# Kernel tuning notes

Hardware: AMD Instinct MI355X
Metric: run time of the kernel (lower is better)

Reference implementation:

```python
import jax, jax.numpy as jnp
import numpy as np

MARGIN = 0.5  # hardcoded in the torch __init__ regardless of the margin arg
P_IDS, K_PER_ID, K_PER_MOD = 32, 8, 4
B, C = P_IDS * K_PER_ID, 1024


def setup_inputs() -> dict:
    key = jax.random.key(0)
    inputs = jax.random.normal(key, (B, C), dtype=jnp.float32)
    # Standard cross-modal ReID sampler: P identities, K instances each,
    # first K/2 from modality 0, last K/2 from modality 1. This guarantees the
    # boolean-mask reshape in the original code is well-formed (M per row).
    targets = jnp.repeat(jnp.arange(P_IDS, dtype=jnp.int32), K_PER_ID)
    subs = jnp.tile(jnp.repeat(jnp.arange(2, dtype=jnp.int32), K_PER_MOD), P_IDS)
    return {"inputs": inputs, "targets": targets, "subs": subs, "m_count": K_PER_MOD}


def _loss(inputs, targets, subs, m_count):
    b, c = inputs.shape
    # Mask construction uses detached inputs in the original (clone().detach()).
    xs = jax.lax.stop_gradient(inputs)
    diff = jnp.abs(xs[:, None, :] - xs[None, :, :])                     # (B,B,C)
    identity_mask = targets[:, None] == targets[None, :]                # (B,B)
    modality_mask = subs[:, None] == subs[None, :]                      # (B,B)
    combined = identity_mask & modality_mask                            # (B,B)

    # diff[combined].reshape(B, M, C): every row has exactly m_count trues;
    # stable argsort recovers the selected column indices in ascending order,
    # matching torch's row-major boolean-mask gather.
    order = jnp.argsort(jnp.where(combined, 0, 1), axis=1)              # stable
    idx = order[:, :m_count]                                            # (B,M)
    modality_diff = jnp.take_along_axis(diff, idx[:, :, None], axis=1)  # (B,M,C)

    mean_md = modality_diff.mean(-1, keepdims=True)                     # (B,M,1)
    m_counts = (modality_diff < mean_md * MARGIN).sum(1)                # (B,C) int
    # mdm[i,j,c] = m_counts[i,c] * m_counts[j,c]  (detached float mask)
    mdm = (m_counts[:, None, :] * m_counts[None, :, :]).astype(inputs.dtype)  # (B,B,C)

    mean_d = diff.mean(-1, keepdims=True)                               # (B,B,1)
    idm = (diff < mean_d * MARGIN).astype(inputs.dtype)                 # (B,B,C)

    # Gradient-carrying pairwise differences (vectorized form of the B-loop).
    d = inputs[:, None, :] - inputs[None, :, :]                         # (B,B,C)
    mod_dist = jnp.sqrt(jnp.maximum(((d * mdm) ** 2).sum(-1), 1e-12))   # (B,B)
    id_dist = jnp.sqrt(jnp.maximum(((d * idm) ** 2).sum(-1), 1e-12))    # (B,B)
    id_dist = jnp.where(identity_mask, jnp.inf, id_dist)                # drop same-id

    per_row = jnp.maximum(mod_dist.max(axis=1) * 10.0 - id_dist.min(axis=1), 0.0)
    return per_row.mean()


def reference(inputs, targets, subs, m_count):
    return _loss(inputs, targets, subs, m_count)
```

## Files before the change

kernel.cpp:

```cpp
#include <hip/hip_runtime.h>
#include <math.h>

#define BB 256
#define CC 1024
#define CC4 (CC/4)
#define MARGIN 0.5f
#define NTILE 64
#define JPT 4
#define NP  128

__global__ __launch_bounds__(64) void mcsq_kernel(
    const float* __restrict__ x, const int* __restrict__ targets,
    const int* __restrict__ subs, const int* __restrict__ m_count_p,
    float* __restrict__ mcsq, float* __restrict__ acc,
    unsigned int* __restrict__ cnt_g)
{
    const int i = blockIdx.x;
    const int lane = threadIdx.x;
    if (i == 0 && lane == 0) { *acc = 0.f; *cnt_g = 0u; }
    const int ti = targets[i], si = subs[i];
    int mc = *m_count_p;
    if (mc > 8) mc = 8;

    unsigned long long masks[4];
    #pragma unroll
    for (int q = 0; q < 4; ++q) {
        const int j = q * 64 + lane;
        masks[q] = __ballot(targets[j] == ti && subs[j] == si);
    }
    int idx[8];
    int cnt = 0;
    for (int q = 0; q < 4 && cnt < mc; ++q) {
        unsigned long long m = masks[q];
        while (m && cnt < mc) {
            const int b = __ffsll(m) - 1;
            idx[cnt++] = q * 64 + b;
            m &= m - 1;
        }
    }
    for (int q = 0; q < 4 && cnt < mc; ++q) {
        unsigned long long m = ~masks[q];
        while (m && cnt < mc) {
            const int b = __ffsll(m) - 1;
            idx[cnt++] = q * 64 + b;
            m &= m - 1;
        }
    }

    const float4* x4 = (const float4*)x;
    float4 xi[4];
    #pragma unroll
    for (int t = 0; t < 4; ++t) xi[t] = x4[(long)i * CC4 + lane + 64 * t];

    float4 c4[4];
    #pragma unroll
    for (int t = 0; t < 4; ++t) c4[t] = make_float4(0.f, 0.f, 0.f, 0.f);

    for (int k = 0; k < cnt; ++k) {
        float4 ad[4];
        float s = 0.f;
        #pragma unroll
        for (int t = 0; t < 4; ++t) {
            const float4 xj = x4[(long)idx[k] * CC4 + lane + 64 * t];
            ad[t].x = fabsf(xi[t].x - xj.x);
            ad[t].y = fabsf(xi[t].y - xj.y);
            ad[t].z = fabsf(xi[t].z - xj.z);
            ad[t].w = fabsf(xi[t].w - xj.w);
            s += ad[t].x + ad[t].y + ad[t].z + ad[t].w;
        }
        #pragma unroll
        for (int off = 32; off > 0; off >>= 1) s += __shfl_xor(s, off, 64);
        const float thr = s * (MARGIN / CC);
        #pragma unroll
        for (int t = 0; t < 4; ++t) {
            c4[t].x += (ad[t].x < thr) ? 1.f : 0.f;
            c4[t].y += (ad[t].y < thr) ? 1.f : 0.f;
            c4[t].z += (ad[t].z < thr) ? 1.f : 0.f;
            c4[t].w += (ad[t].w < thr) ? 1.f : 0.f;
        }
    }
    float4* m4 = (float4*)mcsq;
    #pragma unroll
    for (int t = 0; t < 4; ++t) {
        float4 o;
        o.x = c4[t].x * c4[t].x;
        o.y = c4[t].y * c4[t].y;
        o.z = c4[t].z * c4[t].z;
        o.w = c4[t].w * c4[t].w;
        m4[(long)i * CC4 + lane + 64 * t] = o;
    }
}

__global__ __launch_bounds__(256) void pair_kernel(
    const float* __restrict__ x, const float* __restrict__ mcsq,
    const int* __restrict__ targets,
    float* __restrict__ pmax, float* __restrict__ pmin,
    float* __restrict__ pmaxT, float* __restrict__ pminT)
{
    const int tid  = threadIdx.x;
    const int lane = tid & 63;
    const int gw   = blockIdx.x * 4 + (tid >> 6);

    int h = (int)((129.0f - sqrtf(16641.0f - 4.0f * (float)gw)) * 0.5f);
    if (h > 63) h = 63;
    if (h < 0) h = 0;
    while (h > 0 && (129 * h - h * h) > gw) --h;
    while ((129 * (h + 1) - (h + 1) * (h + 1)) <= gw) ++h;
    const int r     = gw - (129 * h - h * h);
    const int cnt_h = 64 - h;
    const int p     = 2 * h + r / cnt_h;
    const int jt    = h + r % cnt_h;

    const int i0 = 2 * p, i1 = 2 * p + 1;

    const float4* x4 = (const float4*)x;
    const float4* m4 = (const float4*)mcsq;

    float4 xi0[4], xi1[4], mi0[4], mi1[4];
    #pragma unroll
    for (int t = 0; t < 4; ++t) {
        const int c4 = lane + 64 * t;
        xi0[t] = x4[(long)i0 * CC4 + c4];
        xi1[t] = x4[(long)i1 * CC4 + c4];
        mi0[t] = m4[(long)i0 * CC4 + c4];
        mi1[t] = m4[(long)i1 * CC4 + c4];
    }
    const int t0 = targets[i0], t1 = targets[i1];

    float max0 = 0.f, max1 = 0.f;
    float min0 = INFINITY, min1 = INFINITY;

    for (int jj = 0; jj < JPT; ++jj) {
        const int j = jt * JPT + jj;
        float4 xa[4], ma[4];
        float s0 = 0.f, s1 = 0.f;
        #pragma unroll
        for (int t = 0; t < 4; ++t) {
            const int c4 = lane + 64 * t;
            xa[t] = x4[(long)j * CC4 + c4];
            ma[t] = m4[(long)j * CC4 + c4];
            s0 += fabsf(xi0[t].x - xa[t].x) + fabsf(xi0[t].y - xa[t].y)
                + fabsf(xi0[t].z - xa[t].z) + fabsf(xi0[t].w - xa[t].w);
            s1 += fabsf(xi1[t].x - xa[t].x) + fabsf(xi1[t].y - xa[t].y)
                + fabsf(xi1[t].z - xa[t].z) + fabsf(xi1[t].w - xa[t].w);
        }
        #pragma unroll
        for (int off = 32; off > 0; off >>= 1) {
            s0 += __shfl_xor(s0, off, 64);
            s1 += __shfl_xor(s1, off, 64);
        }
        const float thr0 = s0 * (MARGIN / CC);
        const float thr1 = s1 * (MARGIN / CC);

        float ids0 = 0.f, ids1 = 0.f, md0 = 0.f, md1 = 0.f;
        #pragma unroll
        for (int t = 0; t < 4; ++t) {
            #pragma unroll
            for (int u = 0; u < 4; ++u) {
                const float xav = (&xa[t].x)[u];
                const float mav = (&ma[t].x)[u];
                const float d0 = (&xi0[t].x)[u] - xav;
                const float q0 = d0 * d0;
                ids0 += (fabsf(d0) < thr0) ? q0 : 0.f;
                md0  += q0 * (&mi0[t].x)[u] * mav;
                const float d1 = (&xi1[t].x)[u] - xav;
                const float q1 = d1 * d1;
                ids1 += (fabsf(d1) < thr1) ? q1 : 0.f;
                md1  += q1 * (&mi1[t].x)[u] * mav;
            }
        }
        #pragma unroll
        for (int off = 32; off > 0; off >>= 1) {
            ids0 += __shfl_xor(ids0, off, 64);
            ids1 += __shfl_xor(ids1, off, 64);
            md0  += __shfl_xor(md0,  off, 64);
            md1  += __shfl_xor(md1,  off, 64);
        }
        const float mod0 = sqrtf(fmaxf(md0, 1e-12f));
        const float mod1 = sqrtf(fmaxf(md1, 1e-12f));
        max0 = fmaxf(max0, mod0);
        max1 = fmaxf(max1, mod1);
        float id0 = sqrtf(fmaxf(ids0, 1e-12f));
        float id1 = sqrtf(fmaxf(ids1, 1e-12f));
        const int tj = targets[j];
        if (tj != t0) min0 = fminf(min0, id0); else id0 = INFINITY;
        if (tj != t1) min1 = fminf(min1, id1); else id1 = INFINITY;
        if (lane == 0) {
            pmaxT[j * NP + p] = fmaxf(mod0, mod1);
            pminT[j * NP + p] = fminf(id0, id1);
        }
    }
    if (lane == 0) {
        pmax[i0 * NTILE + jt] = max0;
        pmax[i1 * NTILE + jt] = max1;
        pmin[i0 * NTILE + jt] = min0;
        pmin[i1 * NTILE + jt] = min1;
    }
}

__global__ __launch_bounds__(64) void final_kernel(
    const float* __restrict__ pmax, const float* __restrict__ pmin,
    const float* __restrict__ pmaxT, const float* __restrict__ pminT,
    float* __restrict__ acc, unsigned int* __restrict__ cnt_g,
    float* __restrict__ out)
{
    const int i = blockIdx.x;
    const int lane = threadIdx.x;
    const int s = i >> 2;
    float mx = 0.f, mn = INFINITY;
    const int t = s + lane;
    if (t < NTILE) {
        mx = fmaxf(mx, pmax[i * NTILE + t]);
        mn = fminf(mn, pmin[i * NTILE + t]);
    }
    const int pv = 2 * s + 2;
    if (lane < pv) {
        mx = fmaxf(mx, pmaxT[i * NP + lane]);
        mn = fminf(mn, pminT[i * NP + lane]);
    }
    if (lane + 64 < pv) {
        mx = fmaxf(mx, pmaxT[i * NP + lane + 64]);
        mn = fminf(mn, pminT[i * NP + lane + 64]);
    }
    #pragma unroll
    for (int off = 32; off > 0; off >>= 1) {
        mx = fmaxf(mx, __shfl_xor(mx, off, 64));
        mn = fminf(mn, __shfl_xor(mn, off, 64));
    }
    if (lane == 0) {
        const float per = fmaxf(mx * 10.f - mn, 0.f);
        atomicAdd(acc, per * (1.0f / BB));
        __threadfence();
        const unsigned int old = atomicAdd(cnt_g, 1u);
        if (old == BB - 1) {
            __threadfence();
            out[0] = atomicAdd(acc, 0.0f);
        }
    }
}

extern "C" void kernel_launch(void* const* d_in, const int* in_sizes, int n_in,
                              void* d_out, int out_size, void* d_ws, size_t ws_size,
                              hipStream_t stream)
{
    const float* x       = (const float*)d_in[0];
    const int*   targets = (const int*)d_in[1];
    const int*   subs    = (const int*)d_in[2];
    const int*   m_count = (const int*)d_in[3];
    float* out  = (float*)d_out;

    float* mcsq  = (float*)d_ws;
    float* pmax  = mcsq  + (long)BB * CC;
    float* pmin  = pmax  + BB * NTILE;
    float* pmaxT = pmin  + BB * NTILE;
    float* pminT = pmaxT + BB * NP;
    float* acc   = pminT + BB * NP;
    unsigned int* cnt_g = (unsigned int*)(acc + 1);

    mcsq_kernel <<<BB,   64, 0, stream>>>(x, targets, subs, m_count, mcsq, acc, cnt_g);
    pair_kernel <<<1040, 256, 0, stream>>>(x, mcsq, targets, pmax, pmin, pmaxT, pminT);
    final_kernel<<<BB,   64, 0, stream>>>(pmax, pmin, pmaxT, pminT, acc, cnt_g, out);
}
```

Measured before the change: 95.57 us.

## Stage j-tile rows in LDS and assign one i-row per wave

The pair kernel's work decomposition changes. Each block now covers a triangular (i-group of 4 rows, j-tile of 4 columns) pair, and each wave handles a single i row instead of two. The four j rows of x and mcsq are loaded cooperatively into 32KB of shared memory, so the four waves reuse them without each fetching them from global memory. The grid doubles to 2080 blocks and the transposed partial buffers grow to BB×BB. The trade is less register reuse of j data across two i rows, in exchange for more parallelism and lower register pressure.

```diff
diff --git a/kernel.cpp b/kernel.cpp
--- a/kernel.cpp
+++ b/kernel.cpp
@@ -7,7 +7,6 @@
 #define MARGIN 0.5f
 #define NTILE 64
 #define JPT 4
-#define NP  128
 
 __global__ __launch_bounds__(64) void mcsq_kernel(
     const float* __restrict__ x, const int* __restrict__ targets,
@@ -99,102 +98,110 @@
 {
     const int tid  = threadIdx.x;
     const int lane = tid & 63;
-    const int gw   = blockIdx.x * 4 + (tid >> 6);
-
-    int h = (int)((129.0f - sqrtf(16641.0f - 4.0f * (float)gw)) * 0.5f);
-    if (h > 63) h = 63;
-    if (h < 0) h = 0;
-    while (h > 0 && (129 * h - h * h) > gw) --h;
-    while ((129 * (h + 1) - (h + 1) * (h + 1)) <= gw) ++h;
-    const int r     = gw - (129 * h - h * h);
-    const int cnt_h = 64 - h;
-    const int p     = 2 * h + r / cnt_h;
-    const int jt    = h + r % cnt_h;
-
-    const int i0 = 2 * p, i1 = 2 * p + 1;
+    const int w    = tid >> 6;
+    const int b    = blockIdx.x;
+
+    int jt = (int)((sqrtf(8.0f * (float)b + 1.0f) - 1.0f) * 0.5f);
+    if (jt < 0) jt = 0;
+    if (jt > 63) jt = 63;
+    while (jt > 0 && (jt * (jt + 1)) / 2 > b) --jt;
+    while (((jt + 1) * (jt + 2)) / 2 <= b) ++jt;
+    const int ig = b - (jt * (jt + 1)) / 2;
+    const int i  = ig * 4 + w;
+    const int j0 = jt * JPT;
+
+    __shared__ float lds[8192];
+    float4* lds4 = (float4*)lds;
 
     const float4* x4 = (const float4*)x;
     const float4* m4 = (const float4*)mcsq;
 
-    float4 xi0[4], xi1[4], mi0[4], mi1[4];
+    const int ti = targets[i];
+    int tj[4];
+    #pragma unroll
+    for (int q = 0; q < 4; ++q) tj[q] = targets[j0 + q];
+
+    float4 xi[4], mi[4];
     #pragma unroll
     for (int t = 0; t < 4; ++t) {
         const int c4 = lane + 64 * t;
-        xi0[t] = x4[(long)i0 * CC4 + c4];
-        xi1[t] = x4[(long)i1 * CC4 + c4];
-        mi0[t] = m4[(long)i0 * CC4 + c4];
-        mi1[t] = m4[(long)i1 * CC4 + c4];
-    }
-    const int t0 = targets[i0], t1 = targets[i1];
-
-    float max0 = 0.f, max1 = 0.f;
-    float min0 = INFINITY, min1 = INFINITY;
-
+        xi[t] = x4[(long)i * CC4 + c4];
+        mi[t] = m4[(long)i * CC4 + c4];
+    }
+
+    {
+        float4 st[8];
+        #pragma unroll
+        for (int q = 0; q < 4; ++q) {
+            st[q]     = x4[(long)(j0 + q) * CC4 + tid];
+            st[4 + q] = m4[(long)(j0 + q) * CC4 + tid];
+        }
+        #pragma unroll
+        for (int q = 0; q < 8; ++q) lds4[q * 256 + tid] = st[q];
+    }
+    __syncthreads();
+
+    const float4* lx = lds4;
+    const float4* lm = lds4 + 1024;
+
+    float mx = 0.f, mn = INFINITY;
+
+    #pragma unroll
     for (int jj = 0; jj < JPT; ++jj) {
-        const int j = jt * JPT + jj;
-        float4 xa[4], ma[4];
-        float s0 = 0.f, s1 = 0.f;
-        #pragma unroll
-        for (int t = 0; t < 4; ++t) {
-            const int c4 = lane + 64 * t;
-            xa[t] = x4[(long)j * CC4 + c4];
-            ma[t] = m4[(long)j * CC4 + c4];
-            s0 += fabsf(xi0[t].x - xa[t].x) + fabsf(xi0[t].y - xa[t].y)
-                + fabsf(xi0[t].z - xa[t].z) + fabsf(xi0[t].w - xa[t].w);
-            s1 += fabsf(xi1[t].x - xa[t].x) + fabsf(xi1[t].y - xa[t].y)
-                + fabsf(xi1[t].z - xa[t].z) + fabsf(xi1[t].w - xa[t].w);
-        }
-        #pragma unroll
-        for (int off = 32; off > 0; off >>= 1) {
-            s0 += __shfl_xor(s0, off, 64);
-            s1 += __shfl_xor(s1, off, 64);
-        }
-        const float thr0 = s0 * (MARGIN / CC);
-        const float thr1 = s1 * (MARGIN / CC);
-
-        float ids0 = 0.f, ids1 = 0.f, md0 = 0.f, md1 = 0.f;
+        const int j = j0 + jj;
+
+        float4 xa[4];
+        float s = 0.f;
+        #pragma unroll
+        for (int t = 0; t < 4; ++t) {
+            xa[t] = lx[jj * 256 + lane + 64 * t];
+            s += fabsf(xi[t].x - xa[t].x) + fabsf(xi[t].y - xa[t].y)
+               + fabsf(xi[t].z - xa[t].z) + fabsf(xi[t].w - xa[t].w);
+        }
+
+        float4 ma[4];
+        #pragma unroll
+        for (int t = 0; t < 4; ++t) ma[t] = lm[jj * 256 + lane + 64 * t];
+
+        #pragma unroll
+        for (int off = 32; off > 0; off >>= 1) s += __shfl_xor(s, off, 64);
+        const float thr = s * (MARGIN / CC);
+
+        float ids = 0.f, md = 0.f;
         #pragma unroll
         for (int t = 0; t < 4; ++t) {
             #pragma unroll
             for (int u = 0; u < 4; ++u) {
+                const float xiv = (&xi[t].x)[u];
+                const float miv = (&mi[t].x)[u];
                 const float xav = (&xa[t].x)[u];
                 const float mav = (&ma[t].x)[u];
-                const float d0 = (&xi0[t].x)[u] - xav;
-                const float q0 = d0 * d0;
-                ids0 += (fabsf(d0) < thr0) ? q0 : 0.f;
-                md0  += q0 * (&mi0[t].x)[u] * mav;
-                const float d1 = (&xi1[t].x)[u] - xav;
-                const float q1 = d1 * d1;
-                ids1 += (fabsf(d1) < thr1) ? q1 : 0.f;
-                md1  += q1 * (&mi1[t].x)[u] * mav;
+                const float d = xiv - xav;
+                const float q = d * d;
+                ids += (fabsf(d) < thr) ? q : 0.f;
+                md  += q * miv * mav;
             }
         }
         #pragma unroll
         for (int off = 32; off > 0; off >>= 1) {
-            ids0 += __shfl_xor(ids0, off, 64);
-            ids1 += __shfl_xor(ids1, off, 64);
-            md0  += __shfl_xor(md0,  off, 64);
-            md1  += __shfl_xor(md1,  off, 64);
-        }
-        const float mod0 = sqrtf(fmaxf(md0, 1e-12f));
-        const float mod1 = sqrtf(fmaxf(md1, 1e-12f));
-        max0 = fmaxf(max0, mod0);
-        max1 = fmaxf(max1, mod1);
-        float id0 = sqrtf(fmaxf(ids0, 1e-12f));
-        float id1 = sqrtf(fmaxf(ids1, 1e-12f));
-        const int tj = targets[j];
-        if (tj != t0) min0 = fminf(min0, id0); else id0 = INFINITY;
-        if (tj != t1) min1 = fminf(min1, id1); else id1 = INFINITY;
+            ids += __shfl_xor(ids, off, 64);
+            md  += __shfl_xor(md,  off, 64);
+        }
+
+        const float mod = sqrtf(fmaxf(md, 1e-12f));
+        float idv = sqrtf(fmaxf(ids, 1e-12f));
+        mx = fmaxf(mx, mod);
+        if (tj[jj] != ti) mn = fminf(mn, idv); else idv = INFINITY;
+
         if (lane == 0) {
-            pmaxT[j * NP + p] = fmaxf(mod0, mod1);
-            pminT[j * NP + p] = fminf(id0, id1);
-        }
-    }
+            pmaxT[j * BB + i] = mod;
+            pminT[j * BB + i] = idv;
+        }
+    }
+
     if (lane == 0) {
-        pmax[i0 * NTILE + jt] = max0;
-        pmax[i1 * NTILE + jt] = max1;
-        pmin[i0 * NTILE + jt] = min0;
-        pmin[i1 * NTILE + jt] = min1;
+        pmax[i * NTILE + jt] = mx;
+        pmin[i * NTILE + jt] = mn;
     }
 }
 
@@ -213,14 +220,14 @@
         mx = fmaxf(mx, pmax[i * NTILE + t]);
         mn = fminf(mn, pmin[i * NTILE + t]);
     }
-    const int pv = 2 * s + 2;
-    if (lane < pv) {
-        mx = fmaxf(mx, pmaxT[i * NP + lane]);
-        mn = fminf(mn, pminT[i * NP + lane]);
-    }
-    if (lane + 64 < pv) {
-        mx = fmaxf(mx, pmaxT[i * NP + lane + 64]);
-        mn = fminf(mn, pminT[i * NP + lane + 64]);
+    const int pv = 4 * s + 4;
+    #pragma unroll
+    for (int q = 0; q < 4; ++q) {
+        const int c = lane + 64 * q;
+        if (c < pv) {
+            mx = fmaxf(mx, pmaxT[i * BB + c]);
+            mn = fminf(mn, pminT[i * BB + c]);
+        }
     }
     #pragma unroll
     for (int off = 32; off > 0; off >>= 1) {
@@ -253,11 +260,11 @@
     float* pmax  = mcsq  + (long)BB * CC;
     float* pmin  = pmax  + BB * NTILE;
     float* pmaxT = pmin  + BB * NTILE;
-    float* pminT = pmaxT + BB * NP;
-    float* acc   = pminT + BB * NP;
+    float* pminT = pmaxT + BB * BB;
+    float* acc   = pminT + BB * BB;
     unsigned int* cnt_g = (unsigned int*)(acc + 1);
 
     mcsq_kernel <<<BB,   64, 0, stream>>>(x, targets, subs, m_count, mcsq, acc, cnt_g);
-    pair_kernel <<<1040, 256, 0, stream>>>(x, mcsq, targets, pmax, pmin, pmaxT, pminT);
+    pair_kernel <<<2080, 256, 0, stream>>>(x, mcsq, targets, pmax, pmin, pmaxT, pminT);
     final_kernel<<<BB,   64, 0, stream>>>(pmax, pmin, pmaxT, pminT, acc, cnt_g, out);
 }
```

Measured after the change: 89.04 us. -6.8%, faster.

## Process two j-tiles per wave, use DPP reductions, halve pair grid

Applied to the files above, without the earlier changes.

Each wavefront in pair_kernel now handles two consecutive j-tiles instead of one. This reuses the i-row registers (xi, mi) across twice the work and halves the grid from 1040 to 528 blocks, with a new triangular index mapping. Wave reductions replace most shuffle-xor steps with DPP row operations plus readfirstlane, and the mcsq loads are issued after the L1 sum so they overlap. Launch bounds now request 4 blocks per CU. The costs are fewer waves to hide latency and a serial loop to compute the tile index.

```diff
diff --git a/kernel.cpp b/kernel.cpp
--- a/kernel.cpp
+++ b/kernel.cpp
@@ -8,6 +8,22 @@
 #define NTILE 64
 #define JPT 4
 #define NP  128
+
+template<int CTRL>
+__device__ __forceinline__ float dpp_add(float v) {
+    const int pi = __builtin_amdgcn_update_dpp(
+        0, __float_as_int(v), CTRL, 0xF, 0xF, false);
+    return v + __int_as_float(pi);
+}
+__device__ __forceinline__ float wred(float v) {
+    v += __shfl_xor(v, 32, 64);
+    v += __shfl_xor(v, 16, 64);
+    v = dpp_add<0x128>(v);
+    v = dpp_add<0x124>(v);
+    v = dpp_add<0x4E>(v);
+    v = dpp_add<0xB1>(v);
+    return __int_as_float(__builtin_amdgcn_readfirstlane(__float_as_int(v)));
+}
 
 __global__ __launch_bounds__(64) void mcsq_kernel(
     const float* __restrict__ x, const int* __restrict__ targets,
@@ -91,7 +107,7 @@
     }
 }
 
-__global__ __launch_bounds__(256) void pair_kernel(
+__global__ __launch_bounds__(256, 4) void pair_kernel(
     const float* __restrict__ x, const float* __restrict__ mcsq,
     const int* __restrict__ targets,
     float* __restrict__ pmax, float* __restrict__ pmin,
@@ -99,17 +115,19 @@
 {
     const int tid  = threadIdx.x;
     const int lane = tid & 63;
-    const int gw   = blockIdx.x * 4 + (tid >> 6);
-
-    int h = (int)((129.0f - sqrtf(16641.0f - 4.0f * (float)gw)) * 0.5f);
-    if (h > 63) h = 63;
-    if (h < 0) h = 0;
-    while (h > 0 && (129 * h - h * h) > gw) --h;
-    while ((129 * (h + 1) - (h + 1) * (h + 1)) <= gw) ++h;
-    const int r     = gw - (129 * h - h * h);
-    const int cnt_h = 64 - h;
-    const int p     = 2 * h + r / cnt_h;
-    const int jt    = h + r % cnt_h;
+    const int W    = blockIdx.x * 4 + (tid >> 6);
+
+    int h = 0, C = 0;
+    while (true) {
+        const int c2 = 2 * ((65 - h) >> 1);
+        if (C + c2 > W) break;
+        C += c2; ++h;
+    }
+    const int ch  = (65 - h) >> 1;
+    const int r   = W - C;
+    const int p   = 2 * h + ((r >= ch) ? 1 : 0);
+    const int rc  = (r >= ch) ? (r - ch) : r;
+    const int jt0 = h + 2 * rc;
 
     const int i0 = 2 * p, i1 = 2 * p + 1;
 
@@ -127,74 +145,78 @@
     }
     const int t0 = targets[i0], t1 = targets[i1];
 
-    float max0 = 0.f, max1 = 0.f;
-    float min0 = INFINITY, min1 = INFINITY;
-
-    for (int jj = 0; jj < JPT; ++jj) {
-        const int j = jt * JPT + jj;
-        float4 xa[4], ma[4];
-        float s0 = 0.f, s1 = 0.f;
-        #pragma unroll
-        for (int t = 0; t < 4; ++t) {
-            const int c4 = lane + 64 * t;
-            xa[t] = x4[(long)j * CC4 + c4];
-            ma[t] = m4[(long)j * CC4 + c4];
-            s0 += fabsf(xi0[t].x - xa[t].x) + fabsf(xi0[t].y - xa[t].y)
-                + fabsf(xi0[t].z - xa[t].z) + fabsf(xi0[t].w - xa[t].w);
-            s1 += fabsf(xi1[t].x - xa[t].x) + fabsf(xi1[t].y - xa[t].y)
-                + fabsf(xi1[t].z - xa[t].z) + fabsf(xi1[t].w - xa[t].w);
-        }
-        #pragma unroll
-        for (int off = 32; off > 0; off >>= 1) {
-            s0 += __shfl_xor(s0, off, 64);
-            s1 += __shfl_xor(s1, off, 64);
-        }
-        const float thr0 = s0 * (MARGIN / CC);
-        const float thr1 = s1 * (MARGIN / CC);
-
-        float ids0 = 0.f, ids1 = 0.f, md0 = 0.f, md1 = 0.f;
-        #pragma unroll
-        for (int t = 0; t < 4; ++t) {
+    #pragma unroll
+    for (int q = 0; q < 2; ++q) {
+        const int jt = jt0 + q;
+        if (jt > 63) break;
+
+        float max0 = 0.f, max1 = 0.f;
+        float min0 = INFINITY, min1 = INFINITY;
+
+        #pragma unroll
+        for (int jj = 0; jj < JPT; ++jj) {
+            const int j = jt * JPT + jj;
+
+            float4 xa[4], ma[4];
+            float s0 = 0.f, s1 = 0.f;
             #pragma unroll
-            for (int u = 0; u < 4; ++u) {
-                const float xav = (&xa[t].x)[u];
-                const float mav = (&ma[t].x)[u];
-                const float d0 = (&xi0[t].x)[u] - xav;
-                const float q0 = d0 * d0;
-                ids0 += (fabsf(d0) < thr0) ? q0 : 0.f;
-                md0  += q0 * (&mi0[t].x)[u] * mav;
-                const float d1 = (&xi1[t].x)[u] - xav;
-                const float q1 = d1 * d1;
-                ids1 += (fabsf(d1) < thr1) ? q1 : 0.f;
-                md1  += q1 * (&mi1[t].x)[u] * mav;
+            for (int t = 0; t < 4; ++t) {
+                const int c4 = lane + 64 * t;
+                xa[t] = x4[(long)j * CC4 + c4];
+                s0 += fabsf(xi0[t].x - xa[t].x) + fabsf(xi0[t].y - xa[t].y)
+                    + fabsf(xi0[t].z - xa[t].z) + fabsf(xi0[t].w - xa[t].w);
+                s1 += fabsf(xi1[t].x - xa[t].x) + fabsf(xi1[t].y - xa[t].y)
+                    + fabsf(xi1[t].z - xa[t].z) + fabsf(xi1[t].w - xa[t].w);
             }
-        }
-        #pragma unroll
-        for (int off = 32; off > 0; off >>= 1) {
-            ids0 += __shfl_xor(ids0, off, 64);
-            ids1 += __shfl_xor(ids1, off, 64);
-            md0  += __shfl_xor(md0,  off, 64);
-            md1  += __shfl_xor(md1,  off, 64);
-        }
-        const float mod0 = sqrtf(fmaxf(md0, 1e-12f));
-        const float mod1 = sqrtf(fmaxf(md1, 1e-12f));
-        max0 = fmaxf(max0, mod0);
-        max1 = fmaxf(max1, mod1);
-        float id0 = sqrtf(fmaxf(ids0, 1e-12f));
-        float id1 = sqrtf(fmaxf(ids1, 1e-12f));
-        const int tj = targets[j];
-        if (tj != t0) min0 = fminf(min0, id0); else id0 = INFINITY;
-        if (tj != t1) min1 = fminf(min1, id1); else id1 = INFINITY;
+            #pragma unroll
+            for (int t = 0; t < 4; ++t)
+                ma[t] = m4[(long)j * CC4 + lane + 64 * t];
+
+            const float thr0 = wred(s0) * (MARGIN / CC);
+            const float thr1 = wred(s1) * (MARGIN / CC);
+
+            float ids0 = 0.f, ids1 = 0.f, md0 = 0.f, md1 = 0.f;
+            #pragma unroll
+            for (int t = 0; t < 4; ++t) {
+                #pragma unroll
+                for (int u = 0; u < 4; ++u) {
+                    const float xav = (&xa[t].x)[u];
+                    const float mav = (&ma[t].x)[u];
+                    const float d0 = (&xi0[t].x)[u] - xav;
+                    const float q0 = d0 * d0;
+                    ids0 += (fabsf(d0) < thr0) ? q0 : 0.f;
+                    md0  += q0 * (&mi0[t].x)[u] * mav;
+                    const float d1 = (&xi1[t].x)[u] - xav;
+                    const float q1 = d1 * d1;
+                    ids1 += (fabsf(d1) < thr1) ? q1 : 0.f;
+                    md1  += q1 * (&mi1[t].x)[u] * mav;
+                }
+            }
+            const float rds0 = wred(ids0);
+            const float rds1 = wred(ids1);
+            const float rmd0 = wred(md0);
+            const float rmd1 = wred(md1);
+
+            const float mod0 = sqrtf(fmaxf(rmd0, 1e-12f));
+            const float mod1 = sqrtf(fmaxf(rmd1, 1e-12f));
+            max0 = fmaxf(max0, mod0);
+            max1 = fmaxf(max1, mod1);
+            float id0 = sqrtf(fmaxf(rds0, 1e-12f));
+            float id1 = sqrtf(fmaxf(rds1, 1e-12f));
+            const int tj = targets[j];
+            if (tj != t0) min0 = fminf(min0, id0); else id0 = INFINITY;
+            if (tj != t1) min1 = fminf(min1, id1); else id1 = INFINITY;
+            if (lane == 0) {
+                pmaxT[j * NP + p] = fmaxf(mod0, mod1);
+                pminT[j * NP + p] = fminf(id0, id1);
+            }
+        }
         if (lane == 0) {
-            pmaxT[j * NP + p] = fmaxf(mod0, mod1);
-            pminT[j * NP + p] = fminf(id0, id1);
-        }
-    }
-    if (lane == 0) {
-        pmax[i0 * NTILE + jt] = max0;
-        pmax[i1 * NTILE + jt] = max1;
-        pmin[i0 * NTILE + jt] = min0;
-        pmin[i1 * NTILE + jt] = min1;
+            pmax[i0 * NTILE + jt] = max0;
+            pmax[i1 * NTILE + jt] = max1;
+            pmin[i0 * NTILE + jt] = min0;
+            pmin[i1 * NTILE + jt] = min1;
+        }
     }
 }
 
@@ -257,7 +279,7 @@
     float* acc   = pminT + BB * NP;
     unsigned int* cnt_g = (unsigned int*)(acc + 1);
 
-    mcsq_kernel <<<BB,   64, 0, stream>>>(x, targets, subs, m_count, mcsq, acc, cnt_g);
-    pair_kernel <<<1040, 256, 0, stream>>>(x, mcsq, targets, pmax, pmin, pmaxT, pminT);
-    final_kernel<<<BB,   64, 0, stream>>>(pmax, pmin, pmaxT, pminT, acc, cnt_g, out);
-}
+    mcsq_kernel <<<BB,  64, 0, stream>>>(x, targets, subs, m_count, mcsq, acc, cnt_g);
+    pair_kernel <<<528, 256, 0, stream>>>(x, mcsq, targets, pmax, pmin, pmaxT, pminT);
+    final_kernel<<<BB,  64, 0, stream>>>(pmax, pmin, pmaxT, pminT, acc, cnt_g, out);
+}
```

Result: slower. 109.3 us (+14.4%).
